# Kernel optimization log

Hardware: AMD Instinct MI355X
Metric: run time of the kernel (lower is better)

## Reference

```python
import jax, jax.numpy as jnp
import numpy as np

D_MODEL = 1024
NHEAD = 16
HEAD_DIM = D_MODEL // NHEAD
ROPE_BASE = 10000.0


def rotate_half(x):
    h = x.shape[-1] // 2
    return jnp.concatenate((-x[..., h:], x[..., :h]), axis=-1)


def rope_cos_sin(seq_len, dim, dtype):
    inv_freq = 1.0 / (ROPE_BASE ** (jnp.arange(0, dim, 2, dtype=jnp.float32) / dim))
    t = jnp.arange(seq_len, dtype=jnp.float32)
    freqs = jnp.einsum('i,j->ij', t, inv_freq)  # [S, dim/2]
    emb = jnp.concatenate((freqs, freqs), axis=-1)  # [S, dim]
    return jnp.cos(emb).astype(dtype), jnp.sin(emb).astype(dtype)


def setup_inputs() -> dict:
    key = jax.random.key(0)
    ks = jax.random.split(key, 9)
    b, s = 2, 2048
    lim = 1.0 / np.sqrt(D_MODEL)
    def lin(kw, kb):
        W = jax.random.uniform(kw, (D_MODEL, D_MODEL), jnp.float32, -lim, lim)
        bia = jax.random.uniform(kb, (D_MODEL,), jnp.float32, -lim, lim)
        return W, bia
    Wq, bq = lin(ks[0], ks[1])
    Wk, bk = lin(ks[2], ks[3])
    Wv, bv = lin(ks[4], ks[5])
    Wo, bo = lin(ks[6], ks[7])
    x = jax.random.normal(ks[8], (b, s, D_MODEL), jnp.float32)
    return {"x": x, "Wq": Wq, "bq": bq, "Wk": Wk, "bk": bk,
            "Wv": Wv, "bv": bv, "Wo": Wo, "bo": bo}


def reference(x, Wq, bq, Wk, bk, Wv, bv, Wo, bo):
    b, s, _ = x.shape
    scale = jnp.sqrt(jnp.asarray(HEAD_DIM, x.dtype))
    # projections (torch Linear: y = x @ W.T + b)
    q = x @ Wq.T + bq
    k = x @ Wk.T + bk
    v = x @ Wv.T + bv
    # [b, h, s, d]
    def split_heads(t):
        return t.reshape(b, s, NHEAD, HEAD_DIM).transpose(0, 2, 1, 3)
    q, k, v = split_heads(q), split_heads(k), split_heads(v)
    cos, sin = rope_cos_sin(s, HEAD_DIM, x.dtype)  # [s, d]
    q = q * cos + rotate_half(q) * sin
    k = k * cos + rotate_half(k) * sin
    scores = jnp.einsum('bhqd,bhkd->bhqk', q, k) / scale
    probs = jax.nn.softmax(scores, axis=-1)
    out = jnp.einsum('bhqk,bhkd->bhqd', probs, v)
    out = out.transpose(0, 2, 1, 3).reshape(b, s, D_MODEL)
    return out @ Wo.T + bo
```

## Files before the change

### kernel.cpp

```cpp
#include <hip/hip_runtime.h>
#include <hip/hip_bf16.h>
#include <stdint.h>


typedef __attribute__((ext_vector_type(8))) short bf16x8;
typedef __attribute__((ext_vector_type(4))) float f32x4;
typedef __attribute__((ext_vector_type(16))) float f32x16;
typedef __attribute__((ext_vector_type(4))) short short4v;
typedef __attribute__((ext_vector_type(4))) float float4v;
typedef __attribute__((ext_vector_type(4))) unsigned uint32x4;

#define DEV __device__ __forceinline__

DEV short f2bf(float f) {
  union { float f; uint32_t u; } v; v.f = f;
  uint32_t r = (v.u + 0x7fffu + ((v.u >> 16) & 1u)) >> 16;
  return (short)(uint16_t)r;
}
DEV float bf2f(short b) {
  union { uint32_t u; float f; } v; v.u = ((uint32_t)(uint16_t)b) << 16;
  return v.f;
}
DEV unsigned cvtpk(float a, float b) {
  unsigned d;
  asm("v_cvt_pk_bf16_f32 %0, %1, %2" : "=v"(d) : "v"(a), "v"(b));
  return d;
}
DEV void gload16(const void* g, const void* l) {
  __builtin_amdgcn_global_load_lds((const __attribute__((address_space(1))) void*)g,
                                   (__attribute__((address_space(3))) void*)l, 16, 0, 0);
}

__global__ void convert_kernel(const float* __restrict__ x,
                               const float* __restrict__ wq, const float* __restrict__ wk,
                               const float* __restrict__ wv, const float* __restrict__ wo,
                               short* __restrict__ xb, short* __restrict__ wqb,
                               short* __restrict__ wkb, short* __restrict__ wvb,
                               short* __restrict__ wob) {
  const int idx = blockIdx.x * blockDim.x + threadIdx.x;
  const float* src; short* dst; int off;
  if (idx < 1048576)      { src = x;  dst = xb;  off = idx; }
  else if (idx < 1310720) { src = wq; dst = wqb; off = idx - 1048576; }
  else if (idx < 1572864) { src = wk; dst = wkb; off = idx - 1310720; }
  else if (idx < 1835008) { src = wv; dst = wvb; off = idx - 1572864; }
  else                    { src = wo; dst = wob; off = idx - 1835008; }
  float4v v = *(const float4v*)(src + (size_t)off * 4);
  short4v o;
  o[0] = f2bf(v[0]); o[1] = f2bf(v[1]); o[2] = f2bf(v[2]); o[3] = f2bf(v[3]);
  *(short4v*)(dst + (size_t)off * 4) = o;
}

__global__ void rope_table_kernel(float* __restrict__ ct, float* __restrict__ st) {
  const int idx = blockIdx.x * blockDim.x + threadIdx.x;
  const int t = idx >> 5, j = idx & 31;
  const float f = (float)t * exp2f(-(float)j * (13.287712379549449f / 32.f));
  ct[idx] = cosf(f);
  st[idx] = sinf(f);
}

template<bool FINAL>
__global__ __launch_bounds__(256, 2) void gemm_bt(
    const short* __restrict__ A,
    const short* __restrict__ W0, const short* __restrict__ W1, const short* __restrict__ W2,
    const float* __restrict__ b0, const float* __restrict__ b1, const float* __restrict__ b2,
    short* __restrict__ o0, short* __restrict__ o1, short* __restrict__ o2,
    float* __restrict__ of,
    const float* __restrict__ ct, const float* __restrict__ st) {
  constexpr int K = 1024;
  __shared__ short lds[2 * 128 * 64];
  short* As = lds;
  short* Ws = lds + 128 * 64;

  const int tid = threadIdx.x;
  const int lane = tid & 63;
  const int w = tid >> 6;
  const int wr = w >> 1, wc = w & 1;
  const int bn = blockIdx.x, bm = blockIdx.y, z = blockIdx.z;

  const short* Wt = (z == 0) ? W0 : (z == 1 ? W1 : W2);
  const float* bias = (z == 0) ? b0 : (z == 1 ? b1 : b2);
  short* ob = (z == 0) ? o0 : (z == 1 ? o1 : o2);

  const int lrow = lane >> 3;
  const int clog = 16 * ((lane & 7) ^ lrow);

  f32x4 acc[4][4] = {};
  const size_t arowbase = (size_t)(bm * 128) * K;
  const size_t wrowbase = (size_t)(bn * 128) * K;

  for (int kt = 0; kt < K / 64; ++kt) {
    __syncthreads();
#pragma unroll
    for (int i = 0; i < 4; ++i) {
      const int c = i * 4 + w;
      const int row = c * 8 + lrow;
      gload16(A + arowbase + (size_t)row * K + kt * 64 + (clog >> 1),
              (const char*)As + c * 1024);
      gload16(Wt + wrowbase + (size_t)row * K + kt * 64 + (clog >> 1),
              (const char*)Ws + c * 1024);
    }
    __syncthreads();
#pragma unroll
    for (int kk = 0; kk < 2; ++kk) {
      bf16x8 af[4], bf[4];
      const int kb = (kk * 32 + (lane >> 4) * 8) * 2;
#pragma unroll
      for (int mi = 0; mi < 4; ++mi) {
        const int row = wr * 64 + mi * 16 + (lane & 15);
        af[mi] = *(const bf16x8*)((const char*)As + row * 128 + (kb ^ ((row & 7) << 4)));
      }
#pragma unroll
      for (int ni = 0; ni < 4; ++ni) {
        const int row = wc * 64 + ni * 16 + (lane & 15);
        bf[ni] = *(const bf16x8*)((const char*)Ws + row * 128 + (kb ^ ((row & 7) << 4)));
      }
#pragma unroll
      for (int mi = 0; mi < 4; ++mi)
#pragma unroll
        for (int ni = 0; ni < 4; ++ni)
          acc[mi][ni] = __builtin_amdgcn_mfma_f32_16x16x32_bf16(af[mi], bf[ni], acc[mi][ni], 0, 0, 0);
    }
  }

  float bv[4];
#pragma unroll
  for (int ni = 0; ni < 4; ++ni)
    bv[ni] = bias[bn * 128 + wc * 64 + ni * 16 + (lane & 15)];

#pragma unroll
  for (int mi = 0; mi < 4; ++mi) {
#pragma unroll
    for (int r = 0; r < 4; ++r) {
      const int m = bm * 128 + wr * 64 + mi * 16 + (lane >> 4) * 4 + r;
      float v[4];
#pragma unroll
      for (int ni = 0; ni < 4; ++ni) v[ni] = acc[mi][ni][r] + bv[ni];
      if (!FINAL && z < 2) {
        const int s = m & 2047;
        const float sc = (z == 0) ? 0.18033688011f : 1.0f;
#pragma unroll
        for (int jj = 0; jj < 2; ++jj) {
          const int j = jj * 16 + (lane & 15);
          const float c = ct[s * 32 + j] * sc, sn = st[s * 32 + j] * sc;
          const float a = v[jj], bb = v[jj + 2];
          v[jj]     = a * c - bb * sn;
          v[jj + 2] = bb * c + a * sn;
        }
      }
#pragma unroll
      for (int ni = 0; ni < 4; ++ni) {
        const int n = bn * 128 + wc * 64 + ni * 16 + (lane & 15);
        if (FINAL) {
          of[(size_t)m * 1024 + n] = v[ni];
        } else {
          const int b = m >> 11, s = m & 2047, h = n >> 6, d = n & 63;
          ob[(((size_t)(b * 16 + h)) * 2048 + s) * 64 + d] = f2bf(v[ni]);
        }
      }
    }
  }
}

__global__ void vtrans_kernel(const short* __restrict__ v, short* __restrict__ vt) {
  __shared__ short t[64][72];
  const int bh = blockIdx.x, st0 = blockIdx.y * 64;
  const int tid = threadIdx.x;
#pragma unroll
  for (int i = 0; i < 2; ++i) {
    const int j = i * 256 + tid;
    const int row = j >> 3, c8 = (j & 7) * 8;
    *(bf16x8*)&t[row][c8] = *(const bf16x8*)(v + (((size_t)bh * 2048) + st0 + row) * 64 + c8);
  }
  __syncthreads();
#pragma unroll
  for (int i = 0; i < 2; ++i) {
    const int j = i * 256 + tid;
    const int dd = j >> 3, s8 = (j & 7) * 8;
    const int b16 = s8 & ~15;
    const int hi8 = (s8 >> 3) & 1;
    bf16x8 o;
#pragma unroll
    for (int e = 0; e < 8; ++e)
      o[e] = t[b16 + 4 * hi8 + (e & 3) + 8 * (e >> 2)][dd];
    *(bf16x8*)(vt + (((size_t)bh * 64) + dd) * 2048 + st0 + s8) = o;
  }
}

__global__ __launch_bounds__(256, 2) void attn_kernel(
    const short* __restrict__ q, const short* __restrict__ k,
    const short* __restrict__ vt, short* __restrict__ ao) {
  __shared__ char ldsb[65536];

  const int tid = threadIdx.x, lane = tid & 63, w = tid >> 6;
  const int wg = w & 1, g = w >> 1;
  const int hi = lane >> 5;
  const int bh = blockIdx.x, qt = blockIdx.y;
  const int lrow = lane >> 3;
  const int cshort = 8 * ((lane & 7) ^ lrow);

  const int qrow = qt * 64 + wg * 32 + (lane & 31);
  const short* qb = q + ((size_t)bh * 2048 + qrow) * 64 + hi * 8;
  bf16x8 qf[4];
#pragma unroll
  for (int m = 0; m < 4; ++m) qf[m] = *(const bf16x8*)(qb + 16 * m);

  bf16x8 ones;
#pragma unroll
  for (int j = 0; j < 8; ++j) ones[j] = (short)0x3F80;

  f32x16 acc[2] = {};
  f32x16 lacc = {};

  char* gbase = ldsb + g * 32768;
  const size_t kvoff = (size_t)g * 1024;

  const short* kp = k + ((size_t)bh * 2048 + kvoff + (wg * 4) * 8 + lrow) * 64 + cshort;
  const short* vp[4];
#pragma unroll
  for (int i = 0; i < 4; ++i)
    vp[i] = vt + ((size_t)bh * 64 + (wg * 4 + i) * 8 + lrow) * 2048 + kvoff + cshort;

#pragma unroll
  for (int i = 0; i < 4; ++i) {
    gload16(kp + i * 512, gbase + (wg * 4 + i) * 1024);
    gload16(vp[i], gbase + 8192 + (wg * 4 + i) * 1024);
  }
  kp += 4096;
#pragma unroll
  for (int i = 0; i < 4; ++i) vp[i] += 64;
  __syncthreads();

  int cur = 0;
  for (int j = 0; j < 16; ++j) {
    if (j < 15) {
      char* nb = gbase + (cur ^ 1) * 16384;
#pragma unroll
      for (int i = 0; i < 4; ++i) {
        gload16(kp + i * 512, nb + (wg * 4 + i) * 1024);
        gload16(vp[i], nb + 8192 + (wg * 4 + i) * 1024);
      }
      kp += 4096;
#pragma unroll
      for (int i = 0; i < 4; ++i) vp[i] += 64;
    }

    const char* kb_ = gbase + cur * 16384;
    const char* vb_ = kb_ + 8192;

    f32x16 stv[2] = {};
#pragma unroll
    for (int m = 0; m < 4; ++m) {
      const int bc = 32 * m + 16 * hi;
#pragma unroll
      for (int t = 0; t < 2; ++t) {
        const int row = t * 32 + (lane & 31);
        bf16x8 kf = *(const bf16x8*)(kb_ + row * 128 + (bc ^ ((row & 7) << 4)));
        stv[t] = __builtin_amdgcn_mfma_f32_32x32x16_bf16(kf, qf[m], stv[t], 0, 0, 0);
      }
    }

#pragma unroll
    for (int t = 0; t < 2; ++t)
#pragma unroll
      for (int r = 0; r < 16; ++r)
        stv[t][r] = __builtin_amdgcn_exp2f(stv[t][r]);

#pragma unroll
    for (int sg = 0; sg < 4; ++sg) {
      const int t = sg >> 1, sl = sg & 1;
      uint32x4 pu;
#pragma unroll
      for (int jj = 0; jj < 4; ++jj)
        pu[jj] = cvtpk(stv[t][8 * sl + 2 * jj], stv[t][8 * sl + 2 * jj + 1]);
      bf16x8 pv8 = __builtin_bit_cast(bf16x8, pu);
      const int base = 64 * t + 32 * sl + 16 * hi;
#pragma unroll
      for (int db = 0; db < 2; ++db) {
        const int row = db * 32 + (lane & 31);
        const int sw = (row & 7) << 4;
        bf16x8 vv = *(const bf16x8*)(vb_ + row * 128 + (base ^ sw));
        acc[db] = __builtin_amdgcn_mfma_f32_32x32x16_bf16(vv, pv8, acc[db], 0, 0, 0);
      }
      lacc = __builtin_amdgcn_mfma_f32_32x32x16_bf16(ones, pv8, lacc, 0, 0, 0);
    }

    __syncthreads();
    cur ^= 1;
  }

  float* fm = (float*)(void*)ldsb + wg * 2112;
  if (g == 1) {
    fm[lane] = lacc[0];
#pragma unroll
    for (int db = 0; db < 2; ++db)
#pragma unroll
      for (int r = 0; r < 16; ++r)
        fm[64 + (db * 16 + r) * 64 + lane] = acc[db][r];
  }
  __syncthreads();

  if (g == 0) {
    const float rl = 1.0f / (lacc[0] + fm[lane]);
    const int b = bh >> 4, h = bh & 15;
    short* orow = ao + ((size_t)b * 2048 + qrow) * 1024 + h * 64;
#pragma unroll
    for (int db = 0; db < 2; ++db)
#pragma unroll
      for (int gq = 0; gq < 4; ++gq) {
        short4v o;
#pragma unroll
        for (int jj = 0; jj < 4; ++jj) {
          const int r = 4 * gq + jj;
          const float v1 = fm[64 + (db * 16 + r) * 64 + lane];
          o[jj] = f2bf((acc[db][r] + v1) * rl);
        }
        *(short4v*)(orow + db * 32 + 8 * gq + 4 * hi) = o;
      }
  }
}

extern "C" void kernel_launch(void* const* d_in, const int* in_sizes, int n_in,
                              void* d_out, int out_size, void* d_ws, size_t ws_size,
                              hipStream_t stream) {
  const float* x  = (const float*)d_in[0];
  const float* Wq = (const float*)d_in[1];
  const float* bq = (const float*)d_in[2];
  const float* Wk = (const float*)d_in[3];
  const float* bk = (const float*)d_in[4];
  const float* Wv = (const float*)d_in[5];
  const float* bv = (const float*)d_in[6];
  const float* Wo = (const float*)d_in[7];
  const float* bo = (const float*)d_in[8];
  float* out = (float*)d_out;

  char* ws = (char*)d_ws;
  short* xb  = (short*)(ws);
  short* wqb = (short*)(ws + 8388608);
  short* wkb = (short*)(ws + 10485760);
  short* wvb = (short*)(ws + 12582912);
  short* wob = (short*)(ws + 14680064);
  float* ct  = (float*)(ws + 16777216);
  float* st  = (float*)(ws + 17039360);
  short* qb  = (short*)(ws + 17301504);
  short* kb  = (short*)(ws + 25690112);
  short* vb  = (short*)(ws + 34078720);
  short* vtb = (short*)(ws + 42467328);
  short* ab  = (short*)(ws + 50855936);

  convert_kernel<<<dim3(8192), dim3(256), 0, stream>>>(x, Wq, Wk, Wv, Wo, xb, wqb, wkb, wvb, wob);
  rope_table_kernel<<<dim3(256), dim3(256), 0, stream>>>(ct, st);
  gemm_bt<false><<<dim3(8, 32, 3), dim3(256), 0, stream>>>(
      xb, wqb, wkb, wvb, bq, bk, bv, qb, kb, vb, (float*)nullptr, ct, st);
  vtrans_kernel<<<dim3(32, 32), dim3(256), 0, stream>>>(vb, vtb);
  attn_kernel<<<dim3(32, 32), dim3(256), 0, stream>>>(qb, kb, vtb, ab);
  gemm_bt<true><<<dim3(8, 32, 1), dim3(256), 0, stream>>>(
      ab, wob, (short*)nullptr, (short*)nullptr, bo, (float*)nullptr, (float*)nullptr,
      (short*)nullptr, (short*)nullptr, (short*)nullptr, out, ct, st);
}
```

Before: 115.0 us.

## Process two query tiles per wave in attention to reuse K/V loads

Each wave now handles 64 query rows instead of 32, so the block covers 128 queries and the grid halves. Every K and V fragment read from LDS now feeds two MFMAs, which halves LDS traffic and global K/V loads per query. The softmax row sum is now accumulated with scalar adds plus a cross-half shuffle rather than a ones-matrix MFMA. In exchange, register pressure roughly doubles, which may reduce occupancy under the two-blocks launch bound, and there are fewer blocks to spread across the CUs. The end-of-kernel LDS reduction buffers are doubled to match.

```diff
diff --git a/kernel.cpp b/kernel.cpp
--- a/kernel.cpp
+++ b/kernel.cpp
@@ -198,18 +198,17 @@
   const int lrow = lane >> 3;
   const int cshort = 8 * ((lane & 7) ^ lrow);
 
-  const int qrow = qt * 64 + wg * 32 + (lane & 31);
-  const short* qb = q + ((size_t)bh * 2048 + qrow) * 64 + hi * 8;
-  bf16x8 qf[4];
-#pragma unroll
-  for (int m = 0; m < 4; ++m) qf[m] = *(const bf16x8*)(qb + 16 * m);
-
-  bf16x8 ones;
-#pragma unroll
-  for (int j = 0; j < 8; ++j) ones[j] = (short)0x3F80;
-
-  f32x16 acc[2] = {};
-  f32x16 lacc = {};
+  const int qrow0 = qt * 128 + wg * 64 + (lane & 31);
+  const short* qb = q + ((size_t)bh * 2048 + qrow0) * 64 + hi * 8;
+  bf16x8 qf0[4], qf1[4];
+#pragma unroll
+  for (int m = 0; m < 4; ++m) {
+    qf0[m] = *(const bf16x8*)(qb + 16 * m);
+    qf1[m] = *(const bf16x8*)(qb + 32 * 64 + 16 * m);
+  }
+
+  f32x16 acc0[2] = {}, acc1[2] = {};
+  float l0 = 0.f, l1 = 0.f;
 
   char* gbase = ldsb + g * 32768;
   const size_t kvoff = (size_t)g * 1024;
@@ -247,7 +246,7 @@
     const char* kb_ = gbase + cur * 16384;
     const char* vb_ = kb_ + 8192;
 
-    f32x16 stv[2] = {};
+    f32x16 stv0[2] = {}, stv1[2] = {};
 #pragma unroll
     for (int m = 0; m < 4; ++m) {
       const int bc = 32 * m + 16 * hi;
@@ -255,67 +254,93 @@
       for (int t = 0; t < 2; ++t) {
         const int row = t * 32 + (lane & 31);
         bf16x8 kf = *(const bf16x8*)(kb_ + row * 128 + (bc ^ ((row & 7) << 4)));
-        stv[t] = __builtin_amdgcn_mfma_f32_32x32x16_bf16(kf, qf[m], stv[t], 0, 0, 0);
+        stv0[t] = __builtin_amdgcn_mfma_f32_32x32x16_bf16(kf, qf0[m], stv0[t], 0, 0, 0);
+        stv1[t] = __builtin_amdgcn_mfma_f32_32x32x16_bf16(kf, qf1[m], stv1[t], 0, 0, 0);
       }
     }
 
 #pragma unroll
     for (int t = 0; t < 2; ++t)
 #pragma unroll
-      for (int r = 0; r < 16; ++r)
-        stv[t][r] = __builtin_amdgcn_exp2f(stv[t][r]);
-
+      for (int r = 0; r < 16; ++r) {
+        const float p0 = __builtin_amdgcn_exp2f(stv0[t][r]);
+        const float p1 = __builtin_amdgcn_exp2f(stv1[t][r]);
+        stv0[t][r] = p0; l0 += p0;
+        stv1[t][r] = p1; l1 += p1;
+      }
+
+    uint32x4 pu0[4], pu1[4];
 #pragma unroll
     for (int sg = 0; sg < 4; ++sg) {
       const int t = sg >> 1, sl = sg & 1;
-      uint32x4 pu;
-#pragma unroll
-      for (int jj = 0; jj < 4; ++jj)
-        pu[jj] = cvtpk(stv[t][8 * sl + 2 * jj], stv[t][8 * sl + 2 * jj + 1]);
-      bf16x8 pv8 = __builtin_bit_cast(bf16x8, pu);
+#pragma unroll
+      for (int jj = 0; jj < 4; ++jj) {
+        pu0[sg][jj] = cvtpk(stv0[t][8 * sl + 2 * jj], stv0[t][8 * sl + 2 * jj + 1]);
+        pu1[sg][jj] = cvtpk(stv1[t][8 * sl + 2 * jj], stv1[t][8 * sl + 2 * jj + 1]);
+      }
+    }
+
+#pragma unroll
+    for (int sg = 0; sg < 4; ++sg) {
+      const int t = sg >> 1, sl = sg & 1;
+      const bf16x8 pv0 = __builtin_bit_cast(bf16x8, pu0[sg]);
+      const bf16x8 pv1 = __builtin_bit_cast(bf16x8, pu1[sg]);
       const int base = 64 * t + 32 * sl + 16 * hi;
 #pragma unroll
       for (int db = 0; db < 2; ++db) {
         const int row = db * 32 + (lane & 31);
         const int sw = (row & 7) << 4;
         bf16x8 vv = *(const bf16x8*)(vb_ + row * 128 + (base ^ sw));
-        acc[db] = __builtin_amdgcn_mfma_f32_32x32x16_bf16(vv, pv8, acc[db], 0, 0, 0);
-      }
-      lacc = __builtin_amdgcn_mfma_f32_32x32x16_bf16(ones, pv8, lacc, 0, 0, 0);
+        acc0[db] = __builtin_amdgcn_mfma_f32_32x32x16_bf16(vv, pv0, acc0[db], 0, 0, 0);
+        acc1[db] = __builtin_amdgcn_mfma_f32_32x32x16_bf16(vv, pv1, acc1[db], 0, 0, 0);
+      }
     }
 
     __syncthreads();
     cur ^= 1;
   }
 
-  float* fm = (float*)(void*)ldsb + wg * 2112;
+  l0 += __shfl_xor(l0, 32);
+  l1 += __shfl_xor(l1, 32);
+
+  float* fm0 = (float*)(void*)ldsb + (wg * 2 + 0) * 2112;
+  float* fm1 = (float*)(void*)ldsb + (wg * 2 + 1) * 2112;
   if (g == 1) {
-    fm[lane] = lacc[0];
+    fm0[lane] = l0;
+    fm1[lane] = l1;
 #pragma unroll
     for (int db = 0; db < 2; ++db)
 #pragma unroll
-      for (int r = 0; r < 16; ++r)
-        fm[64 + (db * 16 + r) * 64 + lane] = acc[db][r];
+      for (int r = 0; r < 16; ++r) {
+        fm0[64 + (db * 16 + r) * 64 + lane] = acc0[db][r];
+        fm1[64 + (db * 16 + r) * 64 + lane] = acc1[db][r];
+      }
   }
   __syncthreads();
 
   if (g == 0) {
-    const float rl = 1.0f / (lacc[0] + fm[lane]);
     const int b = bh >> 4, h = bh & 15;
-    short* orow = ao + ((size_t)b * 2048 + qrow) * 1024 + h * 64;
-#pragma unroll
-    for (int db = 0; db < 2; ++db)
-#pragma unroll
-      for (int gq = 0; gq < 4; ++gq) {
-        short4v o;
-#pragma unroll
-        for (int jj = 0; jj < 4; ++jj) {
-          const int r = 4 * gq + jj;
-          const float v1 = fm[64 + (db * 16 + r) * 64 + lane];
-          o[jj] = f2bf((acc[db][r] + v1) * rl);
+#pragma unroll
+    for (int s = 0; s < 2; ++s) {
+      float* fm = s ? fm1 : fm0;
+      f32x16* accp = s ? acc1 : acc0;
+      const float rl = 1.0f / ((s ? l1 : l0) + fm[lane]);
+      const int qrow = qrow0 + 32 * s;
+      short* orow = ao + ((size_t)b * 2048 + qrow) * 1024 + h * 64;
+#pragma unroll
+      for (int db = 0; db < 2; ++db)
+#pragma unroll
+        for (int gq = 0; gq < 4; ++gq) {
+          short4v o;
+#pragma unroll
+          for (int jj = 0; jj < 4; ++jj) {
+            const int r = 4 * gq + jj;
+            const float v1 = fm[64 + (db * 16 + r) * 64 + lane];
+            o[jj] = f2bf((accp[db][r] + v1) * rl);
+          }
+          *(short4v*)(orow + db * 32 + 8 * gq + 4 * hi) = o;
         }
-        *(short4v*)(orow + db * 32 + 8 * gq + 4 * hi) = o;
-      }
+    }
   }
 }
 
@@ -352,7 +377,7 @@
   gemm_bt<false><<<dim3(8, 32, 3), dim3(256), 0, stream>>>(
       xb, wqb, wkb, wvb, bq, bk, bv, qb, kb, vb, (float*)nullptr, ct, st);
   vtrans_kernel<<<dim3(32, 32), dim3(256), 0, stream>>>(vb, vtb);
-  attn_kernel<<<dim3(32, 32), dim3(256), 0, stream>>>(qb, kb, vtb, ab);
+  attn_kernel<<<dim3(32, 16), dim3(256), 0, stream>>>(qb, kb, vtb, ab);
   gemm_bt<true><<<dim3(8, 32, 1), dim3(256), 0, stream>>>(
       ab, wob, (short*)nullptr, (short*)nullptr, bo, (float*)nullptr, (float*)nullptr,
       (short*)nullptr, (short*)nullptr, (short*)nullptr, out, ct, st);
```

New measurement: 108.2 us. 5.9% less time.
